# Kernel tuning notes

Hardware: AMD Instinct MI355X
Metric: run time of the kernel (lower is better)

## Reference

```python
import jax, jax.numpy as jnp
import numpy as np

N_LEVELS = 7
N_HEADS = 2
HIDDEN = 128
LP_P = 4.0  # LPPool1d norm


def setup_inputs() -> dict:
    key = jax.random.key(0)
    ks = jax.random.split(key, 9)
    B, S, H = 2048, 200, HIDDEN
    item_seq = jax.random.randint(ks[0], (B, S), 0, 100)
    item_seq_emb = jax.random.normal(ks[1], (B, S, H), dtype=jnp.float32)
    item_seq_len = jax.random.randint(ks[2], (B,), 0, S)
    scale = 0.02
    W_lq = jax.random.normal(ks[3], (H, H), dtype=jnp.float32) * scale
    b_lq = jnp.zeros((H,), dtype=jnp.float32)
    Wq = jax.random.normal(ks[4], (H, H), dtype=jnp.float32) * scale
    bq = jnp.zeros((H,), dtype=jnp.float32)
    Wk = jax.random.normal(ks[5], (H, H), dtype=jnp.float32) * scale
    bk = jnp.zeros((H,), dtype=jnp.float32)
    return {"item_seq": item_seq, "item_seq_emb": item_seq_emb,
            "item_seq_len": item_seq_len, "W_lq": W_lq, "b_lq": b_lq,
            "Wq": Wq, "bq": bq, "Wk": Wk, "bk": bk}


def reference(item_seq, item_seq_emb, item_seq_len, W_lq, b_lq, Wq, bq, Wk, bk):
    B, S, H = item_seq_emb.shape
    nh, L = N_HEADS, N_LEVELS
    d = H // nh
    mask = item_seq > 0  # [B,S]

    # multi-level gather of last j+1 positions; torch clamp(-1) + index -1 == last pos
    j = jnp.arange(L)
    idx = jnp.clip(item_seq_len[:, None] - (j[None, :] + 1), -1, 1000)  # [B,L]
    idx = jnp.where(idx < 0, idx + S, idx)
    gathered = jnp.take_along_axis(item_seq_emb, idx[:, :, None], axis=1)  # [B,L,H]
    level_emb = jnp.cumsum(gathered, axis=1)  # level i = sum of gathers 0..i

    # shared level-query linear (ModuleList([lin]*L) aliases one Linear)
    queries = level_emb @ W_lq.T + b_lq  # [B,L,H]

    # raw torch .view() reshapes replicated exactly
    q = (queries @ Wq.T + bq).reshape(B * nh, L, d)
    k = (item_seq_emb @ Wk.T + bk).reshape(B * nh, S, d)
    v = item_seq_emb.reshape(B, S, nh, d)

    alpha = jax.nn.sigmoid(jnp.einsum('bld,bsd->bls', q, k))  # [B*nh, L, S]
    alpha = alpha.reshape(B, nh * L, S).transpose(0, 2, 1)  # [B, S, nh*L]
    alpha = jax.nn.softmax(alpha, axis=1)

    # LPPool1d(p=4, kernel=L, stride=L) over last dim -> [B,S,nh]
    alpha = alpha.reshape(B, S, nh, L)
    alpha = jnp.sum(alpha ** LP_P, axis=-1) ** (1.0 / LP_P)

    alpha = jnp.where(mask[:, :, None], alpha, -jnp.inf)
    alpha = jax.nn.softmax(alpha, axis=1)  # dropout off (inference)

    weighted = (alpha[..., None] * v).reshape(B, S, H) * mask[:, :, None].astype(item_seq_emb.dtype)
    return jnp.sum(weighted, axis=1)  # [B,H]
```

## Files before the change

kernel.cpp:

```cpp
#include <hip/hip_runtime.h>
#include <hip/hip_bf16.h>

#define SEQ 200
#define HID 128
#define NLVL 7

#define WS_M16_W 0
#define WS_BF    32768
#define WS_VB    33280
#define WS_CB    33792
#define WS_WC    33796
#define WS_BC    50180
#define WS_WORDS 50308

#define WS_QK    51200
#define QK_STRIDE 4112

#define SCST 212

typedef __attribute__((ext_vector_type(8))) short short8;
typedef __attribute__((ext_vector_type(4))) float f32x4;

__device__ __forceinline__ float bf_lo(unsigned u) { return __uint_as_float(u << 16); }
__device__ __forceinline__ float bf_hi(unsigned u) { return __uint_as_float(u & 0xffff0000u); }
__device__ __forceinline__ unsigned short bf_bits(float f) {
    __hip_bfloat16 h = __float2bfloat16(f);
    return *reinterpret_cast<unsigned short*>(&h);
}
__device__ __forceinline__ unsigned pack_bf(float a, float b) {
    return (unsigned)bf_bits(a) | ((unsigned)bf_bits(b) << 16);
}
__device__ __forceinline__ short8 cvt8(float4 a, float4 b) {
    short8 f;
    f[0] = (short)bf_bits(a.x); f[1] = (short)bf_bits(a.y);
    f[2] = (short)bf_bits(a.z); f[3] = (short)bf_bits(a.w);
    f[4] = (short)bf_bits(b.x); f[5] = (short)bf_bits(b.y);
    f[6] = (short)bf_bits(b.z); f[7] = (short)bf_bits(b.w);
    return f;
}

__global__ __launch_bounds__(256) void precomp0(
    const float* __restrict__ Wlq, const float* __restrict__ blq,
    const float* __restrict__ Wq,  const float* __restrict__ bq,
    float* __restrict__ ws)
{
    int id = blockIdx.x * 256 + threadIdx.x;
    int r = id >> 7, j = id & 127;
    float acc = 0.f;
    #pragma unroll 8
    for (int c = 0; c < 128; ++c) acc += Wq[r * 128 + c] * Wlq[c * 128 + j];
    ws[WS_WC + id] = acc;
    if (id < 128) {
        float b = bq[id];
        #pragma unroll 8
        for (int c = 0; c < 128; ++c) b += Wq[id * 128 + c] * blq[c];
        ws[WS_BC + id] = b;
    }
}

__global__ __launch_bounds__(256) void precomp1(
    const float* __restrict__ Wk, const float* __restrict__ bk, float* __restrict__ ws)
{
    int gid = blockIdx.x * 256 + threadIdx.x;
    if (gid < 65536) {
        int j = gid & 127, c = (gid >> 7) & 127, g = gid >> 14;
        int u = g >> 1, par = g & 1;
        const float* wc = ws + WS_WC + u * 64 * 128 + j;
        const float* wk = Wk + par * 64 * 128 + c;
        float acc = 0.f;
        #pragma unroll 8
        for (int d = 0; d < 64; ++d) acc += wc[d * 128] * wk[d * 128];
        ((__hip_bfloat16*)ws)[gid] = __float2bfloat16(acc);
    } else if (gid < 66048) {
        int t = gid - 65536, c = t & 127, g = t >> 7;
        int u = g >> 1, par = g & 1;
        float acc = 0.f;
        #pragma unroll 8
        for (int d = 0; d < 64; ++d)
            acc += ws[WS_BC + u * 64 + d] * Wk[(par * 64 + d) * 128 + c];
        ws[WS_BF + t] = acc;
    } else if (gid < 66560) {
        int t = gid - 66048, j = t & 127, g = t >> 7;
        int u = g >> 1, par = g & 1;
        float acc = 0.f;
        #pragma unroll 8
        for (int d = 0; d < 64; ++d)
            acc += ws[WS_WC + (u * 64 + d) * 128 + j] * bk[par * 64 + d];
        ws[WS_VB + t] = acc;
    } else if (gid < 66564) {
        int g = gid - 66560, u = g >> 1, par = g & 1;
        float acc = 0.f;
        for (int d = 0; d < 64; ++d)
            acc += ws[WS_BC + u * 64 + d] * bk[par * 64 + d];
        ws[WS_CB + g] = acc;
    }
}

__global__ __launch_bounds__(512, 8) void precomp2(
    const float* __restrict__ emb, const int* __restrict__ seq_len,
    float* __restrict__ ws)
{
    const int b    = blockIdx.x;
    const int tid  = threadIdx.x;
    const int wave = tid >> 6, lane = tid & 63;
    const int ln   = lane & 15, quad = lane >> 4;

    __shared__ __align__(16) float s_lvl[NLVL * 128];
    __shared__ __align__(16) short s_lvl16[16 * 136];

    unsigned* wq = (unsigned*)ws + WS_QK + (size_t)b * QK_STRIDE;
    const float* embb = emb + (size_t)b * SEQ * HID;
    const int len = seq_len[b];

    if (tid < HID) {
        float e[NLVL];
        #pragma unroll
        for (int j = 0; j < NLVL; ++j) {
            int idx = len - (j + 1);
            if (idx < 0) idx = SEQ - 1;
            e[j] = embb[(size_t)idx * HID + tid];
        }
        float acc = 0.f;
        #pragma unroll
        for (int j = 0; j < NLVL; ++j) {
            acc += e[j];
            s_lvl[j * HID + tid] = acc;
            s_lvl16[j * 136 + tid] = (short)bf_bits(acc);
        }
    } else if (tid >= 448) {
        int t = tid - 448;
        for (int i = t; i < 136; i += 64) {
            wq[1904 + i] = 0u;
            wq[3944 + i] = 0u;
        }
    }
    __syncthreads();

    {
        const int g = wave >> 1, halfm = wave & 1;
        const int mrow = ln;
        short8 bfrag[4];
        #pragma unroll
        for (int k = 0; k < 4; ++k)
            bfrag[k] = *(const short8*)(s_lvl16 + mrow * 136 + k * 32 + quad * 8);
        const short* M16 = (const short*)ws;
        #pragma unroll
        for (int mt = 0; mt < 4; ++mt) {
            int mtile = halfm * 4 + mt;
            int cbase = mtile * 16 + quad * 4;
            f32x4 acc;
            #pragma unroll
            for (int r = 0; r < 4; ++r) acc[r] = ws[WS_BF + g * 128 + cbase + r];
            const short* Ab = M16 + (g * 128 + mtile * 16 + mrow) * 128;
            #pragma unroll
            for (int k = 0; k < 4; ++k) {
                short8 afrag = *(const short8*)(Ab + k * 32 + quad * 8);
                acc = __builtin_amdgcn_mfma_f32_16x16x32_bf16(afrag, bfrag[k], acc, 0, 0, 0);
            }
            if (mrow < NLVL) {
                int qrow = mrow * 4 + g;
                unsigned h01 = pack_bf(acc[0], acc[1]);
                unsigned h23 = pack_bf(acc[2], acc[3]);
                float l0 = acc[0] - bf_lo(h01), l1 = acc[1] - bf_hi(h01);
                float l2 = acc[2] - bf_lo(h23), l3 = acc[3] - bf_hi(h23);
                int woff = qrow * 68 + mtile * 8 + quad * 2;
                *(uint2*)(wq + woff)        = make_uint2(h01, h23);
                *(uint2*)(wq + 2040 + woff) = make_uint2(pack_bf(l0, l1), pack_bf(l2, l3));
            }
        }
        if (tid < 448) {
            int grp = tid >> 4, sub = tid & 15;
            int gg = grp & 3, L = grp >> 2;
            const float* vb = ws + WS_VB + gg * 128;
            const float* lv = s_lvl + L * 128;
            float acc = 0.f;
            #pragma unroll
            for (int k = 0; k < 8; ++k) {
                int j = sub + 16 * k;
                acc += lv[j] * vb[j];
            }
            acc += __shfl_xor(acc, 1, 16);
            acc += __shfl_xor(acc, 2, 16);
            acc += __shfl_xor(acc, 4, 16);
            acc += __shfl_xor(acc, 8, 16);
            if (sub == 0) ((float*)(wq + 4080))[grp] = acc + ws[WS_CB + gg];
        }
    }
}

__global__ __launch_bounds__(512, 8) void mixer_main(
    const int* __restrict__ item_seq,
    const float* __restrict__ emb,
    const float* __restrict__ ws,
    float* __restrict__ out)
{
    const int b    = blockIdx.x;
    const int tid  = threadIdx.x;
    const int wave = tid >> 6, lane = tid & 63;
    const int ln   = lane & 15, quad = lane >> 4;

    __shared__ __align__(16) unsigned s_qkbuf[4108];
    __shared__ __align__(16) float s_scores[14 * SCST];
    __shared__ float s_denom[14];
    __shared__ __align__(16) float s_A[2 * SEQ];
    __shared__ __align__(16) float s_red[512];

    short* s_qkhi = (short*)s_qkbuf;
    float* s_qb   = (float*)(s_qkbuf + 4080);

    const float* embb = emb + (size_t)b * SEQ * HID;
    const unsigned* qsrc = (const unsigned*)ws + WS_QK + (size_t)b * QK_STRIDE;

    {
        const uint4* src = (const uint4*)qsrc;
        uint4* dst = (uint4*)s_qkbuf;
        for (int i = tid; i < 1027; i += 512) dst[i] = src[i];
        if (tid < 14) s_denom[tid] = 0.f;
    }
    __syncthreads();

    {
        #pragma unroll 1
        for (int t = wave; t < 14; t += 8) {
            const int h = t / 7, mtile = t % 7;
            int gqrow = mtile * 16 + ln;
            int rowg = h * 100 + (gqrow < 100 ? gqrow : 99);
            const float* Arow = embb + (size_t)rowg * HID;
            float qbv = (ln < 14) ? s_qb[h * 14 + ln] : 0.f;
            f32x4 acc;
            acc[0] = qbv; acc[1] = qbv; acc[2] = qbv; acc[3] = qbv;
            #pragma unroll 2
            for (int kk = 0; kk < 4; ++kk) {
                float4 v0 = *(const float4*)(Arow + kk * 32 + quad * 8);
                float4 v1 = *(const float4*)(Arow + kk * 32 + quad * 8 + 4);
                short8 afrag = cvt8(v0, v1);
                const int boff = (h * 14 + ln) * 136 + kk * 32 + quad * 8;
                short8 bhi = *(const short8*)(s_qkhi + boff);
                short8 blo = *(const short8*)(s_qkhi + 2040 * 2 + boff);
                acc = __builtin_amdgcn_mfma_f32_16x16x32_bf16(afrag, bhi, acc, 0, 0, 0);
                acc = __builtin_amdgcn_mfma_f32_16x16x32_bf16(afrag, blo, acc, 0, 0, 0);
            }
            float part = 0.f;
            if (ln < 14) {
                int srow = (h * 7 + (ln >> 1)) * SCST, par = ln & 1;
                #pragma unroll
                for (int i = 0; i < 4; ++i) {
                    int gq = mtile * 16 + quad * 4 + i;
                    if (gq < 100) {
                        float sg = 1.f / (1.f + __expf(-acc[i]));
                        float E = __expf(sg);
                        s_scores[srow + 2 * gq + par] = E;
                        part += E;
                    }
                }
            }
            part += __shfl_xor(part, 16, 64);
            part += __shfl_xor(part, 32, 64);
            part += __shfl_xor(part, 1, 64);
            if (quad == 0 && ln < 14 && (ln & 1) == 0)
                atomicAdd(&s_denom[h * 7 + (ln >> 1)], part);
        }
    }
    __syncthreads();

    if (tid < 2 * SEQ) {
        int h = tid / SEQ, s2 = tid % SEQ;
        float ssum = 0.f;
        #pragma unroll
        for (int l = 0; l < NLVL; ++l) {
            float v = __fdividef(s_scores[(h * NLVL + l) * SCST + s2],
                                 s_denom[h * NLVL + l]);
            float v2 = v * v;
            ssum += v2 * v2;
        }
        float A = sqrtf(sqrtf(ssum));
        int m = item_seq[(size_t)b * SEQ + s2];
        s_A[tid] = (m > 0) ? __expf(A) : 0.f;
    }
    __syncthreads();

    {
        int c = tid & 127, qq = tid >> 7;
        int h = c >> 6;
        const float* wv = s_A + h * SEQ + qq * 50;
        const float* eg = embb + (size_t)(qq * 50) * HID + c;
        float acc = 0.f;
        #pragma unroll 10
        for (int s = 0; s < 50; ++s)
            acc += wv[s] * eg[(size_t)s * HID];
        s_red[tid] = acc;
    }
    __syncthreads();

    if (tid < HID) {
        int h = tid >> 6;
        const float* row = s_A + h * SEQ;
        float sum = row[lane] + row[lane + 64] + row[lane + 128]
                  + ((lane + 192 < 200) ? row[lane + 192] : 0.f);
        #pragma unroll
        for (int mm = 1; mm < 64; mm <<= 1) sum += __shfl_xor(sum, mm, 64);
        float inv = 1.f / sum;
        float tot = (s_red[tid] + s_red[tid + 128] + s_red[tid + 256] + s_red[tid + 384]) * inv;
        out[(size_t)b * HID + tid] = tot;
    }
}

__global__ __launch_bounds__(256) void mixer_fallback(
    const int* __restrict__ item_seq, const float* __restrict__ emb,
    const int* __restrict__ seq_len,
    const float* __restrict__ Wlq, const float* __restrict__ blq,
    const float* __restrict__ Wq,  const float* __restrict__ bq,
    const float* __restrict__ Wk,  const float* __restrict__ bk,
    float* __restrict__ out)
{
    const int b = blockIdx.x, tid = threadIdx.x;
    __shared__ unsigned s_embu[SEQ * 65];
    __shared__ float s_qk[28 * 128];
    __shared__ float s_qb[28];
    __shared__ float s_tmp[2800];
    __shared__ float s_A[400];
    __shared__ float s_red[256];
    __shared__ float s_inv[2];

    {
        const float4* src = (const float4*)(emb + (size_t)b * SEQ * HID);
        for (int i = tid; i < SEQ * 32; i += 256) {
            int row = i >> 5, j = i & 31;
            float4 v = src[i];
            unsigned* dst = s_embu + row * 65 + 2 * j;
            dst[0] = pack_bf(v.x, v.y);
            dst[1] = pack_bf(v.z, v.w);
        }
    }
    const int len = seq_len[b];
    if (tid < HID) {
        float acc = 0.f;
        for (int j = 0; j < NLVL; ++j) {
            int idx = len - (j + 1);
            if (idx < 0) idx = SEQ - 1;
            acc += emb[(size_t)b * SEQ * HID + (size_t)idx * HID + tid];
            s_tmp[j * HID + tid] = acc;
        }
    }
    __syncthreads();
    for (int t = tid; t < NLVL * HID; t += 256) {
        int l = t >> 7, c = t & 127;
        const float* x = s_tmp + l * HID;
        float acc = blq[c];
        #pragma unroll 8
        for (int k = 0; k < HID; ++k) acc += x[k] * Wlq[c * HID + k];
        s_tmp[896 + t] = acc;
    }
    __syncthreads();
    for (int t = tid; t < NLVL * HID; t += 256) {
        int l = t >> 7, c = t & 127;
        const float* x = s_tmp + 896 + l * HID;
        float acc = bq[c];
        #pragma unroll 8
        for (int k = 0; k < HID; ++k) acc += x[k] * Wq[c * HID + k];
        s_tmp[t] = acc;
    }
    __syncthreads();
    for (int o = tid; o < 28 * 128; o += 256) {
        int qrow = o >> 7, c = o & 127;
        int hl = qrow >> 1, par = qrow & 1;
        const float* qv = s_tmp + hl * 64;
        float acc = 0.f;
        #pragma unroll 8
        for (int d2 = 0; d2 < 64; ++d2) acc += qv[d2] * Wk[(par * 64 + d2) * HID + c];
        s_qk[qrow * 128 + c] = acc;
    }
    if (tid < 28) {
        int hl = tid >> 1, par = tid & 1;
        float acc = 0.f;
        for (int d2 = 0; d2 < 64; ++d2) acc += s_tmp[hl * 64 + d2] * bk[par * 64 + d2];
        s_qb[tid] = acc;
    }
    __syncthreads();
    for (int o = tid; o < 700; o += 256) {
        int hl = o / 50, g = o % 50;
        int h = (hl >= 7) ? 1 : 0;
        int rA = h * 100 + g, rB = rA + 50;
        const unsigned* eA = s_embu + rA * 65;
        const unsigned* eB = s_embu + rB * 65;
        const float* k0 = s_qk + (hl * 2) * 128;
        const float* k1 = s_qk + (hl * 2 + 1) * 128;
        float a0 = 0.f, a1 = 0.f, c0a = 0.f, c1a = 0.f;
        #pragma unroll 4
        for (int kk = 0; kk < 64; ++kk) {
            unsigned uA = eA[kk], uB = eB[kk];
            float2 w0 = *(const float2*)(k0 + 2 * kk);
            float2 w1 = *(const float2*)(k1 + 2 * kk);
            float alo = bf_lo(uA), ahi = bf_hi(uA);
            float blo = bf_lo(uB), bhi = bf_hi(uB);
            a0 += alo * w0.x + ahi * w0.y;  a1 += alo * w1.x + ahi * w1.y;
            c0a += blo * w0.x + bhi * w0.y; c1a += blo * w1.x + bhi * w1.y;
        }
        float qb0 = s_qb[hl * 2], qb1 = s_qb[hl * 2 + 1];
        float* row = s_tmp + hl * 200;
        row[2 * g]       = 1.f / (1.f + __expf(-(a0 + qb0)));
        row[2 * g + 1]   = 1.f / (1.f + __expf(-(a1 + qb1)));
        row[2 * g + 100] = 1.f / (1.f + __expf(-(c0a + qb0)));
        row[2 * g + 101] = 1.f / (1.f + __expf(-(c1a + qb1)));
    }
    __syncthreads();
    const int wave = tid >> 6, lane = tid & 63;
    for (int r = wave; r < 14; r += 4) {
        float* row = s_tmp + r * 200;
        float e0 = __expf(row[lane]), e1 = __expf(row[lane + 64]);
        float e2 = __expf(row[lane + 128]);
        float e3 = (lane + 192 < 200) ? __expf(row[lane + 192]) : 0.f;
        float sum = e0 + e1 + e2 + e3;
        #pragma unroll
        for (int m = 1; m < 64; m <<= 1) sum += __shfl_xor(sum, m, 64);
        float inv = 1.f / sum;
        row[lane] = e0 * inv; row[lane + 64] = e1 * inv; row[lane + 128] = e2 * inv;
        if (lane + 192 < 200) row[lane + 192] = e3 * inv;
    }
    __syncthreads();
    for (int o = tid; o < 2 * SEQ; o += 256) {
        int h = o / SEQ, s2 = o % SEQ;
        float ssum = 0.f;
        #pragma unroll
        for (int l = 0; l < NLVL; ++l) {
            float v = s_tmp[(h * NLVL + l) * 200 + s2];
            float v2 = v * v; ssum += v2 * v2;
        }
        float A = sqrtf(sqrtf(ssum));
        s_A[o] = (item_seq[(size_t)b * SEQ + s2] > 0) ? __expf(A) : 0.f;
    }
    __syncthreads();
    if (wave < 2) {
        const float* row = s_A + wave * SEQ;
        float sum = row[lane] + row[lane + 64] + row[lane + 128]
                  + ((lane + 192 < 200) ? row[lane + 192] : 0.f);
        #pragma unroll
        for (int m = 1; m < 64; m <<= 1) sum += __shfl_xor(sum, m, 64);
        if (lane == 0) s_inv[wave] = 1.f / sum;
    }
    __syncthreads();
    {
        int c = tid & 127, halfb = tid >> 7;
        int h = c >> 6;
        const float* wv = s_A + h * SEQ + halfb * 100;
        float acc = 0.f;
        #pragma unroll 4
        for (int s2 = 0; s2 < 100; ++s2) {
            unsigned u = s_embu[(halfb * 100 + s2) * 65 + (c >> 1)];
            acc += wv[s2] * ((c & 1) ? bf_hi(u) : bf_lo(u));
        }
        s_red[tid] = acc;
    }
    __syncthreads();
    if (tid < HID) {
        int h = tid >> 6;
        out[(size_t)b * HID + tid] = (s_red[tid] + s_red[tid + 128]) * s_inv[h];
    }
}

extern "C" void kernel_launch(void* const* d_in, const int* in_sizes, int n_in,
                              void* d_out, int out_size, void* d_ws, size_t ws_size,
                              hipStream_t stream) {
    const int* item_seq = (const int*)d_in[0];
    const float* emb    = (const float*)d_in[1];
    const int* seq_len  = (const int*)d_in[2];
    const float* Wlq    = (const float*)d_in[3];
    const float* blq    = (const float*)d_in[4];
    const float* Wq     = (const float*)d_in[5];
    const float* bq     = (const float*)d_in[6];
    const float* Wk     = (const float*)d_in[7];
    const float* bk     = (const float*)d_in[8];
    float* out          = (float*)d_out;
    const int B = in_sizes[2];

    const size_t need = ((size_t)WS_QK + (size_t)B * QK_STRIDE) * 4;
    if (ws_size >= need) {
        float* ws = (float*)d_ws;
        precomp0<<<64, 256, 0, stream>>>(Wlq, blq, Wq, bq, ws);
        precomp1<<<261, 256, 0, stream>>>(Wk, bk, ws);
        precomp2<<<B, 512, 0, stream>>>(emb, seq_len, ws);
        mixer_main<<<B, 512, 0, stream>>>(item_seq, emb, ws, out);
    } else {
        mixer_fallback<<<B, 256, 0, stream>>>(item_seq, emb, seq_len, Wlq, blq, Wq, bq, Wk, bk, out);
    }
}
```

Before: 370.4 us.

## Fuse per-batch query precompute kernel into main mixer kernel via shared memory

Merges the per-batch precomp2 kernel into mixer_main, so the folded query/key projections (bf16 hi/lo split) and bias terms go straight into LDS instead of a global workspace buffer that is then reloaded. This removes one launch of B blocks, the global write and read of about 16KB per batch, and the workspace size requirement. In exchange the main kernel does the gather and MFMA precompute before its scoring phase. The scores buffer is reused for the level embeddings, so LDS use stays about the same, but the per-block critical path gets longer.

After: 344.5 us. -7.0%, faster.

```diff
diff --git a/kernel.cpp b/kernel.cpp
--- a/kernel.cpp
+++ b/kernel.cpp
@@ -12,9 +12,6 @@
 #define WS_WC    33796
 #define WS_BC    50180
 #define WS_WORDS 50308
-
-#define WS_QK    51200
-#define QK_STRIDE 4112
 
 #define SCST 212
 
@@ -96,19 +93,30 @@
     }
 }
 
-__global__ __launch_bounds__(512, 8) void precomp2(
-    const float* __restrict__ emb, const int* __restrict__ seq_len,
-    float* __restrict__ ws)
+__global__ __launch_bounds__(512, 8) void mixer_main(
+    const int* __restrict__ item_seq,
+    const float* __restrict__ emb,
+    const int* __restrict__ seq_len,
+    const float* __restrict__ ws,
+    float* __restrict__ out)
 {
     const int b    = blockIdx.x;
     const int tid  = threadIdx.x;
     const int wave = tid >> 6, lane = tid & 63;
     const int ln   = lane & 15, quad = lane >> 4;
 
-    __shared__ __align__(16) float s_lvl[NLVL * 128];
-    __shared__ __align__(16) short s_lvl16[16 * 136];
-
-    unsigned* wq = (unsigned*)ws + WS_QK + (size_t)b * QK_STRIDE;
+    __shared__ __align__(16) short s_qkhi[30 * 136];
+    __shared__ __align__(16) short s_qklo[30 * 136];
+    __shared__ __align__(16) char  s_region[14 * SCST * 4];
+    __shared__ float s_qb[28];
+    __shared__ float s_denom[14];
+    __shared__ __align__(16) float s_A[2 * SEQ];
+    __shared__ __align__(16) float s_red[512];
+
+    float* s_scores = (float*)s_region;
+    float* s_lvl    = (float*)s_region;
+    short* s_lvl16  = (short*)(s_region + 3584);
+
     const float* embb = emb + (size_t)b * SEQ * HID;
     const int len = seq_len[b];
 
@@ -127,12 +135,12 @@
             s_lvl[j * HID + tid] = acc;
             s_lvl16[j * 136 + tid] = (short)bf_bits(acc);
         }
-    } else if (tid >= 448) {
-        int t = tid - 448;
-        for (int i = t; i < 136; i += 64) {
-            wq[1904 + i] = 0u;
-            wq[3944 + i] = 0u;
-        }
+    } else if (tid < 196) {
+        int t = tid - 128;
+        ((uint2*)(s_qkhi + 28 * 136))[t] = make_uint2(0u, 0u);
+        ((uint2*)(s_qklo + 28 * 136))[t] = make_uint2(0u, 0u);
+    } else if (tid < 210) {
+        s_denom[tid - 196] = 0.f;
     }
     __syncthreads();
 
@@ -163,9 +171,8 @@
                 unsigned h23 = pack_bf(acc[2], acc[3]);
                 float l0 = acc[0] - bf_lo(h01), l1 = acc[1] - bf_hi(h01);
                 float l2 = acc[2] - bf_lo(h23), l3 = acc[3] - bf_hi(h23);
-                int woff = qrow * 68 + mtile * 8 + quad * 2;
-                *(uint2*)(wq + woff)        = make_uint2(h01, h23);
-                *(uint2*)(wq + 2040 + woff) = make_uint2(pack_bf(l0, l1), pack_bf(l2, l3));
+                *(uint2*)(s_qkhi + qrow * 136 + cbase) = make_uint2(h01, h23);
+                *(uint2*)(s_qklo + qrow * 136 + cbase) = make_uint2(pack_bf(l0, l1), pack_bf(l2, l3));
             }
         }
         if (tid < 448) {
@@ -183,39 +190,8 @@
             acc += __shfl_xor(acc, 2, 16);
             acc += __shfl_xor(acc, 4, 16);
             acc += __shfl_xor(acc, 8, 16);
-            if (sub == 0) ((float*)(wq + 4080))[grp] = acc + ws[WS_CB + gg];
-        }
-    }
-}
-
-__global__ __launch_bounds__(512, 8) void mixer_main(
-    const int* __restrict__ item_seq,
-    const float* __restrict__ emb,
-    const float* __restrict__ ws,
-    float* __restrict__ out)
-{
-    const int b    = blockIdx.x;
-    const int tid  = threadIdx.x;
-    const int wave = tid >> 6, lane = tid & 63;
-    const int ln   = lane & 15, quad = lane >> 4;
-
-    __shared__ __align__(16) unsigned s_qkbuf[4108];
-    __shared__ __align__(16) float s_scores[14 * SCST];
-    __shared__ float s_denom[14];
-    __shared__ __align__(16) float s_A[2 * SEQ];
-    __shared__ __align__(16) float s_red[512];
-
-    short* s_qkhi = (short*)s_qkbuf;
-    float* s_qb   = (float*)(s_qkbuf + 4080);
-
-    const float* embb = emb + (size_t)b * SEQ * HID;
-    const unsigned* qsrc = (const unsigned*)ws + WS_QK + (size_t)b * QK_STRIDE;
-
-    {
-        const uint4* src = (const uint4*)qsrc;
-        uint4* dst = (uint4*)s_qkbuf;
-        for (int i = tid; i < 1027; i += 512) dst[i] = src[i];
-        if (tid < 14) s_denom[tid] = 0.f;
+            if (sub == 0) s_qb[grp] = acc + ws[WS_CB + gg];
+        }
     }
     __syncthreads();
 
@@ -236,7 +212,7 @@
                 short8 afrag = cvt8(v0, v1);
                 const int boff = (h * 14 + ln) * 136 + kk * 32 + quad * 8;
                 short8 bhi = *(const short8*)(s_qkhi + boff);
-                short8 blo = *(const short8*)(s_qkhi + 2040 * 2 + boff);
+                short8 blo = *(const short8*)(s_qklo + boff);
                 acc = __builtin_amdgcn_mfma_f32_16x16x32_bf16(afrag, bhi, acc, 0, 0, 0);
                 acc = __builtin_amdgcn_mfma_f32_16x16x32_bf16(afrag, blo, acc, 0, 0, 0);
             }
@@ -473,13 +449,11 @@
     float* out          = (float*)d_out;
     const int B = in_sizes[2];
 
-    const size_t need = ((size_t)WS_QK + (size_t)B * QK_STRIDE) * 4;
-    if (ws_size >= need) {
+    if (ws_size >= (size_t)WS_WORDS * 4) {
         float* ws = (float*)d_ws;
         precomp0<<<64, 256, 0, stream>>>(Wlq, blq, Wq, bq, ws);
         precomp1<<<261, 256, 0, stream>>>(Wk, bk, ws);
-        precomp2<<<B, 512, 0, stream>>>(emb, seq_len, ws);
-        mixer_main<<<B, 512, 0, stream>>>(item_seq, emb, ws, out);
+        mixer_main<<<B, 512, 0, stream>>>(item_seq, emb, seq_len, ws, out);
     } else {
         mixer_fallback<<<B, 256, 0, stream>>>(item_seq, emb, seq_len, Wlq, blq, Wq, bq, Wk, bk, out);
     }
```
